# Optimization experiments

Hardware: AMD Instinct MI355X
Metric: run time of the kernel (lower is better)

The kernel has to match this reference:

```python
import jax, jax.numpy as jnp
from jax import lax
import numpy as np

VAR0, VAR1 = 0.1, 0.2
K_TOP, T1, T2 = 5, 0.35, 0.5
ALPHA, GAMMA, BETA = 0.25, 2.0, 0.11


def point_form(b):
    # center form (cx,cy,w,h) -> corner form (x1,y1,x2,y2)
    return jnp.concatenate([b[:, :2] - b[:, 2:] / 2, b[:, :2] + b[:, 2:] / 2], axis=-1)


def jaccard(a, b):
    # a: [N,4], b: [P,4] corner boxes -> IoU [N,P]
    lt = jnp.maximum(a[:, None, :2], b[None, :, :2])
    rb = jnp.minimum(a[:, None, 2:], b[None, :, 2:])
    wh = jnp.clip(rb - lt, 0.0)
    inter = wh[..., 0] * wh[..., 1]
    area_a = ((a[:, 2] - a[:, 0]) * (a[:, 3] - a[:, 1]))[:, None]
    area_b = ((b[:, 2] - b[:, 0]) * (b[:, 3] - b[:, 1]))[None, :]
    return inter / (area_a + area_b - inter)


def encode(matched, priors):
    # matched: corner boxes [P,4], priors: center form [P,4]
    g_cxcy = ((matched[:, :2] + matched[:, 2:]) / 2 - priors[:, :2]) / (VAR0 * priors[:, 2:])
    g_wh = jnp.log((matched[:, 2:] - matched[:, :2]) / priors[:, 2:]) / VAR1
    return jnp.concatenate([g_cxcy, g_wh], axis=-1)


def decode(loc, priors):
    cxcy = priors[:, :2] + loc[:, :2] * VAR0 * priors[:, 2:]
    wh = priors[:, 2:] * jnp.exp(loc[:, 2:] * VAR1)
    return jnp.concatenate([cxcy - wh / 2, cxcy + wh / 2], axis=-1)


def _bce_logits(x, t):
    return jnp.maximum(x, 0.0) - x * t + jnp.log1p(jnp.exp(-jnp.abs(x)))


def focal_loss(logits, target, f_iou=None):
    C = logits.shape[-1]
    t = target.reshape(-1, 1)
    keep = (t >= 0.0).astype(logits.dtype)
    t = jnp.maximum(t, 0.0)
    pos = jnp.sum(t > 0.0).astype(logits.dtype)
    x = jnp.take_along_axis(logits.reshape(-1, C), t.astype(jnp.int32), axis=1)
    ce = _bce_logits(x, t)
    a = t * ALPHA + (1.0 - t) * (1.0 - ALPHA)
    p = jax.nn.sigmoid(x)
    pt = jnp.where(t == 1.0, p, 1.0 - p)
    if f_iou is not None:
        a = lax.stop_gradient(f_iou.reshape(-1, 1)) * a
    loss = a * (1.0 - pt) ** GAMMA * ce * keep
    return jnp.sum(loss) / jnp.maximum(pos, 1.0)


def smoothl1_masked(pred, target, mask):
    # equals SmoothL1Loss on the masked rows: sum(elem)/num_rows
    x = jnp.abs(pred - target)
    elem = jnp.where(x >= BETA, x - 0.5 * BETA, 0.5 * x * x / BETA)
    n = jnp.sum(mask).astype(pred.dtype)
    return jnp.sum(elem * mask[..., None].astype(pred.dtype)) / jnp.maximum(n, 1.0)


def match_image(loc_pred, tgt, priors_c, priors_pt):
    N = tgt.shape[0]
    P = priors_c.shape[0]
    truths = tgt[:, :4]
    labels = tgt[:, 4]
    iou = jaccard(truths, priors_pt)  # [N,P]
    bt_score = jnp.max(iou, axis=0)
    bt_idx = jnp.argmax(iou, axis=0).astype(jnp.int32)

    def greedy(_, st):
        m, s, ix = st
        flat = jnp.argmax(m)
        j = (flat // P).astype(jnp.int32)
        i = (flat % P).astype(jnp.int32)
        v = m.ravel()[flat]
        m = m.at[j, :].set(-1.0)
        m = m.at[:, i].set(-1.0)
        return (m, s.at[i].set(v), ix.at[i].set(j))

    _, bt_score, bt_idx = lax.fori_loop(0, N, greedy, (iou, bt_score, bt_idx))

    conf_s1 = labels[bt_idx]
    conf_s1 = jnp.where(bt_score < T1, 0.0, conf_s1)
    loc_s1 = encode(truths[bt_idx], priors_c)

    decoded = decode(lax.stop_gradient(loc_pred), priors_c)
    c_iou = jaccard(truths, decoded)  # [N,P]
    c_bp_score = jnp.max(c_iou, axis=0)
    c_bp_idx = jnp.argmax(c_iou, axis=0).astype(jnp.int32)
    c_iou = c_iou * (c_iou >= T2).astype(c_iou.dtype)
    tk_s, tk_i = lax.top_k(c_iou, K_TOP)  # per-truth top-K priors
    c_score = jnp.zeros_like(c_bp_score)

    def assign(t, st):
        cbi, cs = st
        i = (t // K_TOP).astype(jnp.int32)
        j = t % K_TOP
        p = tk_i[i, j]
        s = tk_s[i, j]
        cond = (conf_s1[p] < 1.0) & (s > 0.0)
        cbi = cbi.at[p].set(jnp.where(cond, i, cbi[p]))
        cs = cs.at[p].set(jnp.where(cond, s, cs[p]))
        return (cbi, cs)

    c_bp_idx, c_score = lax.fori_loop(0, N * K_TOP, assign, (c_bp_idx, c_score))

    loc_s2 = encode(truths[c_bp_idx], priors_c)
    conf_s2 = labels[c_bp_idx]
    conf_s2 = jnp.where(c_score < T2, -1.0, conf_s2)
    ignore = (bt_score < T1) & (c_bp_score >= T2) & (c_score < T2)
    conf_s1 = jnp.where(ignore, -1.0, conf_s1)
    return conf_s1, loc_s1, conf_s2, loc_s2, c_score


def setup_inputs() -> dict:
    key = jax.random.key(0)
    k1, k2, k3, k4, k5, k6 = jax.random.split(key, 6)
    B, P, N, C = 16, 102400, 32, 2
    loc_data = jax.random.normal(k1, (B, P, 4), jnp.float32)
    conf_data = jax.random.normal(k2, (B, P, C), jnp.float32)
    pcxy = jax.random.uniform(k3, (P, 2), jnp.float32, 0.0, 1.0)
    pwh = jax.random.uniform(k4, (P, 2), jnp.float32, 0.02, 0.25)
    priors = jnp.concatenate([pcxy, pwh], axis=-1)
    tcxy = jax.random.uniform(k5, (B, N, 2), jnp.float32, 0.1, 0.9)
    twh = jax.random.uniform(k6, (B, N, 2), jnp.float32, 0.05, 0.3)
    x1 = jnp.clip(tcxy - twh / 2, 0.0, 1.0)
    x2 = jnp.clip(tcxy + twh / 2, 0.0, 1.0)
    targets = jnp.concatenate([x1, x2, jnp.ones((B, N, 1), jnp.float32)], axis=-1)
    return {"loc_data": loc_data, "conf_data": conf_data, "priors": priors, "targets": targets}


def reference(loc_data, conf_data, priors, targets):
    priors_c = lax.stop_gradient(priors)  # torch uses priors.data
    tgts = lax.stop_gradient(targets)     # torch uses targets[idx].data
    priors_pt = point_form(priors_c)
    conf_t, loc_t, cconf_t, cloc_t, cc_score = jax.vmap(
        lambda lp, tg: match_image(lp, tg, priors_c, priors_pt))(loc_data, tgts)
    m1 = conf_t > 0.0
    m2 = cconf_t > 0.0
    n1 = jnp.sum(m1)
    n2 = jnp.sum(m2)
    l1 = smoothl1_masked(loc_data, loc_t, m1)
    l2 = smoothl1_masked(loc_data, cloc_t, m2)
    f1 = focal_loss(conf_data, conf_t, None)
    f2 = focal_loss(conf_data, cconf_t, cc_score)
    loc_loss = jnp.where(n1 > 0, l1, 0.0) + jnp.where(n2 > 0, l2, 0.0)
    cls_loss = jnp.where(n1 > 0, f1, 0.0) + jnp.where(n2 > 0, f2, 0.0)
    none_ = (n1 == 0) & (n2 == 0)
    return (jnp.where(none_, 1e-4, loc_loss), jnp.where(none_, 1e-4, cls_loss))
```

## Files before the change

kernel.cpp:

```cpp
#include <hip/hip_runtime.h>
#include <cstdint>
#include <cstddef>

#define VAR0_ 0.1f
#define VAR1_ 0.2f
#define KTOP_ 5
#define T1_ 0.35f
#define T2_ 0.5f
#define ALPHA_ 0.25f
#define BETA_ 0.11f
#define BS 256
#define BSK 128
#define NSPLIT 16
#define ILP 4

__device__ __forceinline__ float sl1(float d) {
    float x = fabsf(d);
    return (x >= BETA_) ? (x - 0.5f * BETA_) : (0.5f * x * x / BETA_);
}

__global__ void k_fat1(const float4* __restrict__ loc4, const float4* __restrict__ priors4,
                       const float* __restrict__ targets,
                       float4* __restrict__ recs4,
                       float* __restrict__ cand_v, int* __restrict__ cand_i,
                       int* __restrict__ cand_cnt,
                       float* __restrict__ part_max, int* __restrict__ part_arg,
                       int P, int N, int CAP, int bxPP) {
    int b = blockIdx.y;
    int tid = threadIdx.x;
    if (blockIdx.x < bxPP) {
        int base = blockIdx.x * (BSK * ILP) + tid;
        __shared__ float4 tr4[64];
        __shared__ float trA[64];
        __shared__ float trT[64];
        for (int t = tid; t < N; t += BSK) {
            float x1 = targets[(size_t)(b * N + t) * 5 + 0];
            float y1 = targets[(size_t)(b * N + t) * 5 + 1];
            float x2 = targets[(size_t)(b * N + t) * 5 + 2];
            float y2 = targets[(size_t)(b * N + t) * 5 + 3];
            tr4[t] = make_float4(x1, y1, x2, y2);
            float a = (x2 - x1) * (y2 - y1);
            trA[t] = a;
            trT[t] = a * 0.33330f;
        }
        __syncthreads();
        if (base >= P) return;

        int iv[ILP]; int val[ILP];
        float px1[ILP], py1[ILP], px2[ILP], py2[ILP], pa[ILP];
#pragma unroll
        for (int k = 0; k < ILP; k++) {
            int i = base + k * BSK; iv[k] = i; val[k] = (i < P);
            float4 pr = val[k] ? priors4[i] : make_float4(0.f, 0.f, 1.f, 1.f);
            px1[k] = pr.x - pr.z * 0.5f; py1[k] = pr.y - pr.w * 0.5f;
            px2[k] = pr.x + pr.z * 0.5f; py2[k] = pr.y + pr.w * 0.5f;
            pa[k] = (px2[k] - px1[k]) * (py2[k] - py1[k]);
        }
        float bi[ILP], bu[ILP]; int bn[ILP];
#pragma unroll
        for (int k = 0; k < ILP; k++) { bi[k] = -1.f; bu[k] = 1.f; bn[k] = 0; }
#pragma unroll 2
        for (int n = 0; n < N; n++) {
            float4 t4 = tr4[n];
            float ta = trA[n];
#pragma unroll
            for (int k = 0; k < ILP; k++) {
                float lx = fmaxf(t4.x, px1[k]), ly = fmaxf(t4.y, py1[k]);
                float rx = fminf(t4.z, px2[k]), ry = fminf(t4.w, py2[k]);
                float w = fmaxf(rx - lx, 0.f), h = fmaxf(ry - ly, 0.f);
                float inter = w * h, uni = ta + pa[k] - inter;
                bool bet = inter * bu[k] > bi[k] * uni;
                bi[k] = bet ? inter : bi[k]; bu[k] = bet ? uni : bu[k]; bn[k] = bet ? n : bn[k];
            }
        }
        float bv[ILP];
#pragma unroll
        for (int k = 0; k < ILP; k++) bv[k] = bi[k] / bu[k];

        float dx1[ILP], dy1[ILP], dx2[ILP], dy2[ILP], da[ILP], daC[ILP];
#pragma unroll
        for (int k = 0; k < ILP; k++) {
            float4 pr = val[k] ? priors4[iv[k]] : make_float4(0.f, 0.f, 1.f, 1.f);
            float4 lc = val[k] ? loc4[(size_t)b * P + iv[k]] : make_float4(0.f, 0.f, 0.f, 0.f);
            float dcx = pr.x + lc.x * VAR0_ * pr.z;
            float dcy = pr.y + lc.y * VAR0_ * pr.w;
            float dw = pr.z * expf(lc.z * VAR1_);
            float dh = pr.w * expf(lc.w * VAR1_);
            dx1[k] = dcx - dw * 0.5f; dy1[k] = dcy - dh * 0.5f;
            dx2[k] = dcx + dw * 0.5f; dy2[k] = dcy + dh * 0.5f;
            da[k] = (dx2[k] - dx1[k]) * (dy2[k] - dy1[k]);
            daC[k] = da[k] * 0.33330f;
        }
        unsigned long long hm[ILP];
#pragma unroll
        for (int k = 0; k < ILP; k++) hm[k] = 0ull;
#pragma unroll 2
        for (int n = 0; n < N; n++) {
            float4 t4 = tr4[n];
            float tt = trT[n];
#pragma unroll
            for (int k = 0; k < ILP; k++) {
                float lx = fmaxf(t4.x, dx1[k]), ly = fmaxf(t4.y, dy1[k]);
                float rx = fminf(t4.z, dx2[k]), ry = fminf(t4.w, dy2[k]);
                float w = fmaxf(rx - lx, 0.f), h = fmaxf(ry - ly, 0.f);
                float inter = w * h;
                if (inter >= tt + daC[k]) hm[k] |= (1ull << n);
            }
        }
#pragma unroll
        for (int k = 0; k < ILP; k++) {
            if (!val[k]) continue;
            int had = 0;
            unsigned long long m = hm[k];
            while (m) {
                int n = __ffsll((long long)m) - 1;
                m &= m - 1;
                float4 t4 = tr4[n];
                float lx = fmaxf(t4.x, dx1[k]), ly = fmaxf(t4.y, dy1[k]);
                float rx = fminf(t4.z, dx2[k]), ry = fminf(t4.w, dy2[k]);
                float w = fmaxf(rx - lx, 0.f), h = fmaxf(ry - ly, 0.f);
                float inter = w * h;
                float v = inter / (trA[n] + da[k] - inter);
                if (v >= T2_) {
                    had = 1;
                    int pos = atomicAdd(&cand_cnt[b * N + n], 1);
                    if (pos < CAP) {
                        size_t o = (size_t)(b * N + n) * CAP + pos;
                        cand_v[o] = v; cand_i[o] = iv[k];
                    }
                }
            }
            recs4[(size_t)b * P + iv[k]] =
                make_float4(bv[k], __int_as_float(bn[k] | (had << 16)), __int_as_float(0), 0.f);
        }
    } else {
        int idx = blockIdx.x - bxPP;
        int s = idx % NSPLIT, g = idx / NSPLIT;
        int n0 = g * 4;
        int chunk = (P + NSPLIT - 1) / NSPLIT;
        int i0 = s * chunk;
        int i1 = min(P, i0 + chunk);
        float tx1[4], ty1[4], tx2[4], ty2[4], ta[4];
#pragma unroll
        for (int k = 0; k < 4; k++) {
            int n = min(n0 + k, N - 1);
            tx1[k] = targets[(size_t)(b * N + n) * 5 + 0];
            ty1[k] = targets[(size_t)(b * N + n) * 5 + 1];
            tx2[k] = targets[(size_t)(b * N + n) * 5 + 2];
            ty2[k] = targets[(size_t)(b * N + n) * 5 + 3];
            ta[k] = (tx2[k] - tx1[k]) * (ty2[k] - ty1[k]);
        }
        float cI[4], cU[4]; int cX[4];
#pragma unroll
        for (int k = 0; k < 4; k++) { cI[k] = -1.f; cU[k] = 1.f; cX[k] = 0x7fffffff; }
        for (int i = i0 + tid; i < i1; i += BSK) {
            float4 pr = priors4[i];
            float px1 = pr.x - pr.z * 0.5f, py1 = pr.y - pr.w * 0.5f;
            float px2 = pr.x + pr.z * 0.5f, py2 = pr.y + pr.w * 0.5f;
            float pa = (px2 - px1) * (py2 - py1);
#pragma unroll
            for (int k = 0; k < 4; k++) {
                float lx = fmaxf(tx1[k], px1), ly = fmaxf(ty1[k], py1);
                float rx = fminf(tx2[k], px2), ry = fminf(ty2[k], py2);
                float w = fmaxf(rx - lx, 0.f), h = fmaxf(ry - ly, 0.f);
                float inter = w * h;
                float uni = ta[k] + pa - inter;
                bool bet = inter * cU[k] > cI[k] * uni;
                cI[k] = bet ? inter : cI[k]; cU[k] = bet ? uni : cU[k]; cX[k] = bet ? i : cX[k];
            }
        }
        int lane = tid & 63, wid = tid >> 6;
        __shared__ float swv[BSK / 64];
        __shared__ int swi[BSK / 64];
#pragma unroll
        for (int k = 0; k < 4; k++) {
            if (n0 + k >= N) break;
            float bv = cI[k] / cU[k];
            int bx = cX[k];
#pragma unroll
            for (int off = 32; off > 0; off >>= 1) {
                float ov = __shfl_xor(bv, off);
                int oi = __shfl_xor(bx, off);
                if (ov > bv || (ov == bv && oi < bx)) { bv = ov; bx = oi; }
            }
            if (lane == 0) { swv[wid] = bv; swi[wid] = bx; }
            __syncthreads();
            if (tid == 0) {
                float fv = swv[0]; int fi = swi[0];
                for (int wv = 1; wv < BSK / 64; wv++) {
                    if (swv[wv] > fv || (swv[wv] == fv && swi[wv] < fi)) { fv = swv[wv]; fi = swi[wv]; }
                }
                int o = (b * N + (n0 + k)) * NSPLIT + s;
                part_max[o] = fv; part_arg[o] = fi;
            }
            __syncthreads();
        }
    }
}

__global__ void k_fat2(const float4* __restrict__ loc4, const float4* __restrict__ priors4,
                       const float* __restrict__ targets,
                       const float* __restrict__ cand_v, const int* __restrict__ cand_i,
                       const int* __restrict__ cand_cnt,
                       float* __restrict__ tk_s, int* __restrict__ tk_i,
                       const float* __restrict__ part_max, const int* __restrict__ part_arg,
                       float* __restrict__ recs,
                       int P, int N, int CAP) {
    int b = blockIdx.y;
    int tid = threadIdx.x;
    if ((int)blockIdx.x < N) {
        int n = blockIdx.x;
        int row = b * N + n;
        float vals[KTOP_]; int ids[KTOP_];
#pragma unroll
        for (int k = 0; k < KTOP_; k++) { vals[k] = -1.f; ids[k] = 0x7fffffff; }
        int cnt = cand_cnt[row];
        if (cnt <= CAP) {
            for (int k = tid; k < cnt; k += blockDim.x) {
                float cv = cand_v[(size_t)row * CAP + k];
                int ci = cand_i[(size_t)row * CAP + k];
#pragma unroll
                for (int q = 0; q < KTOP_; q++) {
                    bool better = (cv > vals[q]) || ((cv == vals[q]) && (ci < ids[q]));
                    float tv = better ? cv : vals[q]; int ti = better ? ci : ids[q];
                    cv = better ? vals[q] : cv; ci = better ? ids[q] : ci;
                    vals[q] = tv; ids[q] = ti;
                }
            }
        } else {
            float tx1 = targets[(size_t)row * 5 + 0], ty1 = targets[(size_t)row * 5 + 1];
            float tx2 = targets[(size_t)row * 5 + 2], ty2 = targets[(size_t)row * 5 + 3];
            float ta = (tx2 - tx1) * (ty2 - ty1);
            for (int i = tid; i < P; i += blockDim.x) {
                float4 pr = priors4[i];
                size_t bp = (size_t)b * P + i;
                float4 lc = loc4[bp];
                float dcx = pr.x + lc.x * VAR0_ * pr.z;
                float dcy = pr.y + lc.y * VAR0_ * pr.w;
                float dw = pr.z * expf(lc.z * VAR1_);
                float dh = pr.w * expf(lc.w * VAR1_);
                float dx1 = dcx - dw * 0.5f, dy1 = dcy - dh * 0.5f;
                float dx2 = dcx + dw * 0.5f, dy2 = dcy + dh * 0.5f;
                float lx = fmaxf(tx1, dx1), ly = fmaxf(ty1, dy1);
                float rx = fminf(tx2, dx2), ry = fminf(ty2, dy2);
                float w = fmaxf(rx - lx, 0.f), h = fmaxf(ry - ly, 0.f);
                float inter = w * h;
                float uni = ta + (dx2 - dx1) * (dy2 - dy1) - inter;
                if (inter >= uni * 0.4999990f) {
                    float v = inter / uni;
                    if (v >= T2_) {
                        float cv = v; int ci = i;
#pragma unroll
                        for (int q = 0; q < KTOP_; q++) {
                            bool better = (cv > vals[q]) || ((cv == vals[q]) && (ci < ids[q]));
                            float tv = better ? cv : vals[q]; int ti = better ? ci : ids[q];
                            cv = better ? vals[q] : cv; ci = better ? ids[q] : ci;
                            vals[q] = tv; ids[q] = ti;
                        }
                    }
                }
            }
        }
        __shared__ float mv[BS * KTOP_];
        __shared__ int mi[BS * KTOP_];
#pragma unroll
        for (int k = 0; k < KTOP_; k++) { mv[tid * KTOP_ + k] = vals[k]; mi[tid * KTOP_ + k] = ids[k]; }
        __syncthreads();
        for (int s = BS / 2; s > 0; s >>= 1) {
            if (tid < s) {
#pragma unroll
                for (int j = 0; j < KTOP_; j++) {
                    float cv = mv[(tid + s) * KTOP_ + j];
                    int ci = mi[(tid + s) * KTOP_ + j];
#pragma unroll
                    for (int q = 0; q < KTOP_; q++) {
                        bool better = (cv > vals[q]) || ((cv == vals[q]) && (ci < ids[q]));
                        float tv = better ? cv : vals[q]; int ti = better ? ci : ids[q];
                        cv = better ? vals[q] : cv; ci = better ? ids[q] : ci;
                        vals[q] = tv; ids[q] = ti;
                    }
                }
#pragma unroll
                for (int k = 0; k < KTOP_; k++) { mv[tid * KTOP_ + k] = vals[k]; mi[tid * KTOP_ + k] = ids[k]; }
            }
            __syncthreads();
        }
        if (tid == 0) {
#pragma unroll
            for (int k = 0; k < KTOP_; k++) {
                tk_s[(size_t)row * KTOP_ + k] = (vals[k] > 0.f) ? vals[k] : 0.f;
                tk_i[(size_t)row * KTOP_ + k] = (ids[k] == 0x7fffffff) ? 0 : ids[k];
            }
        }
    } else {
        int lane = tid & 63, wid = tid >> 6;
        extern __shared__ unsigned int mask[];
        int maskWords = (P + 31) >> 5;
        for (int w = tid; w < maskWords; w += BS) mask[w] = 0u;

        float rmax = -2.f; int rarg = 0x7fffffff; int alive = 0;
        float tx1 = 0.f, ty1 = 0.f, tx2 = 0.f, ty2 = 0.f, ta = 0.f;
        if (wid == 0 && lane < N) {
            float bv = -2.f; int bi = 0x7fffffff;
            for (int s = 0; s < NSPLIT; s++) {
                int o = (b * N + lane) * NSPLIT + s;
                float v = part_max[o]; int ix = part_arg[o];
                if (v > bv || (v == bv && ix < bi)) { bv = v; bi = ix; }
            }
            rmax = bv; rarg = bi;
            alive = 1;
            tx1 = targets[(size_t)(b * N + lane) * 5 + 0];
            ty1 = targets[(size_t)(b * N + lane) * 5 + 1];
            tx2 = targets[(size_t)(b * N + lane) * 5 + 2];
            ty2 = targets[(size_t)(b * N + lane) * 5 + 3];
            ta = (tx2 - tx1) * (ty2 - ty1);
        }
        __syncthreads();

        for (int it = 0; it < N; it++) {
            int sel = 0;
            if (wid == 0) {
                float v = (lane < N && alive) ? rmax : -3.f;
                int idx = lane;
#pragma unroll
                for (int off = 32; off > 0; off >>= 1) {
                    float ov = __shfl_xor(v, off);
                    int oi = __shfl_xor(idx, off);
                    if (ov > v || (ov == v && oi < idx)) { v = ov; idx = oi; }
                }
                int bj = idx;
                float bv = v;
                sel = __shfl(rarg, bj);
                if (lane == bj) alive = 0;
                if (lane == 0) {
                    float* base = recs + 4 * ((size_t)b * P + sel);
                    int wrd = __float_as_int(base[1]);
                    base[0] = bv;
                    base[1] = __int_as_float((wrd & ~0xFFFF) | bj);
                    mask[sel >> 5] |= (1u << (sel & 31));
                }
            }
            __syncthreads();
            if (wid == 0) {
                unsigned long long coll = __ballot(lane < N && alive && rarg == sel);
                while (coll) {
                    int r = __ffsll((long long)coll) - 1;
                    coll &= coll - 1;
                    float rx1 = __shfl(tx1, r), ry1 = __shfl(ty1, r);
                    float rx2 = __shfl(tx2, r), ry2 = __shfl(ty2, r);
                    float ra = __shfl(ta, r);
                    float n_i = -2.f, n_u = 1.f; int ni = 0x7fffffff;
                    for (int i = lane; i < P; i += 64) {
                        if (mask[i >> 5] & (1u << (i & 31))) continue;
                        float4 pr = priors4[i];
                        float px1 = pr.x - pr.z * 0.5f, py1 = pr.y - pr.w * 0.5f;
                        float px2 = pr.x + pr.z * 0.5f, py2 = pr.y + pr.w * 0.5f;
                        float lx = fmaxf(rx1, px1), ly = fmaxf(ry1, py1);
                        float rx = fminf(rx2, px2), ry = fminf(ry2, py2);
                        float w = fmaxf(rx - lx, 0.f), h = fmaxf(ry - ly, 0.f);
                        float inter = w * h;
                        float uni = ra + (px2 - px1) * (py2 - py1) - inter;
                        bool better = inter * n_u > n_i * uni;
                        n_i = better ? inter : n_i; n_u = better ? uni : n_u; ni = better ? i : ni;
                    }
                    float nv = n_i / n_u;
#pragma unroll
                    for (int off = 32; off > 0; off >>= 1) {
                        float ov = __shfl_xor(nv, off);
                        int oi = __shfl_xor(ni, off);
                        if (ov > nv || (ov == nv && oi < ni)) { nv = ov; ni = oi; }
                    }
                    if (lane == r) { rmax = nv; rarg = ni; }
                }
            }
            __syncthreads();
        }
    }
}

__global__ void k_assign(const float* __restrict__ targets,
                         const float* __restrict__ tk_s, const int* __restrict__ tk_i,
                         float* __restrict__ recs, int P, int N) {
    int b = blockIdx.x;
    int tid = threadIdx.x;
    int T = N * KTOP_;
    __shared__ int sh_p[512];
    __shared__ float sh_s[512];
    __shared__ int sh_c[512];
    if (tid < T) {
        int i = tid / KTOP_, j = tid % KTOP_;
        int p = tk_i[(size_t)(b * N + i) * KTOP_ + j];
        float s = tk_s[(size_t)(b * N + i) * KTOP_ + j];
        const float* base = recs + 4 * ((size_t)b * P + p);
        float bs = base[0];
        int bj = __float_as_int(base[1]) & 0xFFFF;
        float conf1 = (bs < T1_) ? 0.f : targets[(size_t)(b * N + bj) * 5 + 4];
        sh_p[tid] = p; sh_s[tid] = s;
        sh_c[tid] = (conf1 < 1.f && s > 0.f) ? 1 : 0;
    }
    __syncthreads();
    if (tid < T && sh_c[tid]) {
        int p = sh_p[tid];
        bool last = true;
        for (int t2 = tid + 1; t2 < T; t2++) {
            if (sh_c[t2] && sh_p[t2] == p) { last = false; break; }
        }
        if (last) {
            float* base = recs + 4 * ((size_t)b * P + p);
            base[2] = __int_as_float(tid / KTOP_);
            base[3] = sh_s[tid];
        }
    }
}

__global__ void k_loss(const float4* __restrict__ loc4, const float* __restrict__ conf,
                       const float4* __restrict__ priors4, const float* __restrict__ targets,
                       const float4* __restrict__ recs4,
                       double* __restrict__ partials,
                       int P, int N, int C) {
    int b = blockIdx.y;
    int i = blockIdx.x * blockDim.x + threadIdx.x;
    double l1 = 0.0, l2 = 0.0, f1 = 0.0, f2 = 0.0;
    int n1 = 0, n2 = 0;
    if (i < P) {
        size_t bp = (size_t)b * P + i;
        float4 r = recs4[bp];
        float bs = r.x;
        int widx = __float_as_int(r.y);
        int bj = widx & 0xFFFF;
        int hadCand = (widx >> 16) & 1;
        float cs = r.w;
        int cj = (cs > 0.f) ? __float_as_int(r.z) : 0;
        float lab1 = targets[(size_t)(b * N + bj) * 5 + 4];
        float conf1 = (bs < T1_) ? 0.f : lab1;
        if ((bs < T1_) && hadCand && (cs < T2_)) conf1 = -1.f;
        float lab2 = targets[(size_t)(b * N + cj) * 5 + 4];
        float conf2 = (cs < T2_) ? -1.f : lab2;
        bool m1 = conf1 > 0.f, m2 = conf2 > 0.f;
        n1 = m1 ? 1 : 0; n2 = m2 ? 1 : 0;

        if (m1 || m2) {
            float4 pr = priors4[i];
            float pcx = pr.x, pcy = pr.y, pw = pr.z, ph = pr.w;
            float4 lc = loc4[bp];
            float p0 = lc.x, p1 = lc.y, p2 = lc.z, p3 = lc.w;
            if (m1) {
                const float* tb = &targets[(size_t)(b * N + bj) * 5];
                float gx = ((tb[0] + tb[2]) * 0.5f - pcx) / (VAR0_ * pw);
                float gy = ((tb[1] + tb[3]) * 0.5f - pcy) / (VAR0_ * ph);
                float gw = logf((tb[2] - tb[0]) / pw) / VAR1_;
                float gh = logf((tb[3] - tb[1]) / ph) / VAR1_;
                l1 = (double)(sl1(p0 - gx) + sl1(p1 - gy) + sl1(p2 - gw) + sl1(p3 - gh));
            }
            if (m2) {
                const float* tb = &targets[(size_t)(b * N + cj) * 5];
                float gx = ((tb[0] + tb[2]) * 0.5f - pcx) / (VAR0_ * pw);
                float gy = ((tb[1] + tb[3]) * 0.5f - pcy) / (VAR0_ * ph);
                float gw = logf((tb[2] - tb[0]) / pw) / VAR1_;
                float gh = logf((tb[3] - tb[1]) / ph) / VAR1_;
                l2 = (double)(sl1(p0 - gx) + sl1(p1 - gy) + sl1(p2 - gw) + sl1(p3 - gh));
            }
        }
        float x0, x1v;
        if (C == 2) {
            float2 cv2 = ((const float2*)conf)[bp];
            x0 = cv2.x; x1v = cv2.y;
        } else {
            x0 = conf[bp * C + 0]; x1v = conf[bp * C + 1];
        }
        {
            float t = fmaxf(conf1, 0.f);
            float keep = (conf1 >= 0.f) ? 1.f : 0.f;
            float x = (t >= 1.f) ? x1v : x0;
            float ce = fmaxf(x, 0.f) - x * t + log1pf(expf(-fabsf(x)));
            float a = t * ALPHA_ + (1.f - t) * (1.f - ALPHA_);
            float pr_ = 1.f / (1.f + expf(-x));
            float pt = (t == 1.f) ? pr_ : (1.f - pr_);
            float om = 1.f - pt;
            f1 = (double)(a * om * om * ce * keep);
        }
        {
            float t = fmaxf(conf2, 0.f);
            float keep = (conf2 >= 0.f) ? 1.f : 0.f;
            float x = (t >= 1.f) ? x1v : x0;
            float ce = fmaxf(x, 0.f) - x * t + log1pf(expf(-fabsf(x)));
            float a = cs * (t * ALPHA_ + (1.f - t) * (1.f - ALPHA_));
            float pr_ = 1.f / (1.f + expf(-x));
            float pt = (t == 1.f) ? pr_ : (1.f - pr_);
            float om = 1.f - pt;
            f2 = (double)(a * om * om * ce * keep);
        }
    }
    int tid = threadIdx.x;
    int lane = tid & 63, wid = tid >> 6;
#pragma unroll
    for (int off = 32; off > 0; off >>= 1) {
        l1 += __shfl_xor(l1, off);
        l2 += __shfl_xor(l2, off);
        f1 += __shfl_xor(f1, off);
        f2 += __shfl_xor(f2, off);
        n1 += __shfl_xor(n1, off);
        n2 += __shfl_xor(n2, off);
    }
    __shared__ double swd[BS / 64][4];
    __shared__ int swn[BS / 64][2];
    if (lane == 0) {
        swd[wid][0] = l1; swd[wid][1] = l2; swd[wid][2] = f1; swd[wid][3] = f2;
        swn[wid][0] = n1; swn[wid][1] = n2;
    }
    __syncthreads();
    if (tid == 0) {
        double a0 = 0, a1 = 0, a2 = 0, a3 = 0; int b0 = 0, b1 = 0;
        for (int wv = 0; wv < BS / 64; wv++) {
            a0 += swd[wv][0]; a1 += swd[wv][1]; a2 += swd[wv][2]; a3 += swd[wv][3];
            b0 += swn[wv][0]; b1 += swn[wv][1];
        }
        int blk = blockIdx.y * gridDim.x + blockIdx.x;
        partials[(size_t)blk * 6 + 0] = a0;
        partials[(size_t)blk * 6 + 1] = a1;
        partials[(size_t)blk * 6 + 2] = a2;
        partials[(size_t)blk * 6 + 3] = a3;
        partials[(size_t)blk * 6 + 4] = (double)b0;
        partials[(size_t)blk * 6 + 5] = (double)b1;
    }
}

__global__ void k_final(const double* __restrict__ partials, int nPart, float* __restrict__ out) {
    int tid = threadIdx.x;
    double a[6] = {0, 0, 0, 0, 0, 0};
    for (int k = tid; k < nPart; k += BS) {
#pragma unroll
        for (int j = 0; j < 6; j++) a[j] += partials[(size_t)k * 6 + j];
    }
    __shared__ double sd[BS * 6];
#pragma unroll
    for (int j = 0; j < 6; j++) sd[tid * 6 + j] = a[j];
    __syncthreads();
    for (int s = BS / 2; s > 0; s >>= 1) {
        if (tid < s) {
#pragma unroll
            for (int j = 0; j < 6; j++) sd[tid * 6 + j] += sd[(tid + s) * 6 + j];
        }
        __syncthreads();
    }
    if (tid == 0) {
        double L1 = sd[0], L2 = sd[1], F1 = sd[2], F2 = sd[3], N1 = sd[4], N2 = sd[5];
        double l1v = L1 / fmax(N1, 1.0), l2v = L2 / fmax(N2, 1.0);
        double f1v = F1 / fmax(N1, 1.0), f2v = F2 / fmax(N2, 1.0);
        double locl = (N1 > 0 ? l1v : 0.0) + (N2 > 0 ? l2v : 0.0);
        double clsl = (N1 > 0 ? f1v : 0.0) + (N2 > 0 ? f2v : 0.0);
        if (N1 == 0 && N2 == 0) { locl = 1e-4; clsl = 1e-4; }
        out[0] = (float)locl;
        out[1] = (float)clsl;
    }
}

extern "C" void kernel_launch(void* const* d_in, const int* in_sizes, int n_in,
                              void* d_out, int out_size, void* d_ws, size_t ws_size,
                              hipStream_t stream) {
    const float* targets = (const float*)d_in[3];
    const float* conf = (const float*)d_in[1];
    const float4* loc4 = (const float4*)d_in[0];
    const float4* priors4 = (const float4*)d_in[2];

    int P = in_sizes[2] / 4;
    int B = in_sizes[0] / (P * 4);
    int N = in_sizes[3] / (B * 5);
    int C = in_sizes[1] / (B * P);
    const int CAP = 2048;
    size_t BP = (size_t)B * P;

    unsigned char* ws = (unsigned char*)d_ws;
    size_t off = 0;
    auto alloc = [&](size_t bytes) { size_t cur = off; off += (bytes + 255) & ~(size_t)255; return cur; };
    float* recs = (float*)(ws + alloc(BP * 16));
    float* part_max = (float*)(ws + alloc((size_t)B * N * NSPLIT * 4));
    int* part_arg = (int*)(ws + alloc((size_t)B * N * NSPLIT * 4));
    float* tk_s = (float*)(ws + alloc((size_t)B * N * KTOP_ * 4));
    int* tk_i = (int*)(ws + alloc((size_t)B * N * KTOP_ * 4));
    float* cand_v = (float*)(ws + alloc((size_t)B * N * CAP * 4));
    int* cand_i = (int*)(ws + alloc((size_t)B * N * CAP * 4));
    int* cand_cnt = (int*)(ws + alloc((size_t)B * N * 4));
    int bx = (P + BS - 1) / BS;
    double* partials = (double*)(ws + alloc((size_t)bx * B * 6 * 8));
    float* out = (float*)d_out;

    hipMemsetAsync(cand_cnt, 0, (size_t)B * N * 4, stream);

    int bxPP = (P + BSK * ILP - 1) / (BSK * ILP);
    int ngroup = (N + 3) / 4;
    int bxRM = NSPLIT * ngroup;
    k_fat1<<<dim3(bxPP + bxRM, B), BSK, 0, stream>>>(loc4, priors4, targets, (float4*)recs,
                                                     cand_v, cand_i, cand_cnt,
                                                     part_max, part_arg, P, N, CAP, bxPP);

    int maskWords = (P + 31) / 32;
    size_t shmem = (size_t)maskWords * 4;
    k_fat2<<<dim3(N + 1, B), BS, shmem, stream>>>(loc4, priors4, targets,
                                                  cand_v, cand_i, cand_cnt, tk_s, tk_i,
                                                  part_max, part_arg, recs, P, N, CAP);

    k_assign<<<dim3(B), BS, 0, stream>>>(targets, tk_s, tk_i, recs, P, N);
    k_loss<<<dim3(bx, B), BS, 0, stream>>>(loc4, conf, priors4, targets, (const float4*)recs,
                                           partials, P, N, C);
    k_final<<<1, BS, 0, stream>>>(partials, bx * B, out);
}
```

Before: 213.6 us.

## Merge all stages into one cooperative persistent kernel with grid syncs

```diff
diff --git a/kernel.cpp b/kernel.cpp
--- a/kernel.cpp
+++ b/kernel.cpp
@@ -1,6 +1,9 @@
 #include <hip/hip_runtime.h>
+#include <hip/hip_cooperative_groups.h>
 #include <cstdint>
 #include <cstddef>
+
+namespace cg = cooperative_groups;
 
 #define VAR0_ 0.1f
 #define VAR1_ 0.2f
@@ -10,7 +13,6 @@
 #define ALPHA_ 0.25f
 #define BETA_ 0.11f
 #define BS 256
-#define BSK 128
 #define NSPLIT 16
 #define ILP 4
 
@@ -19,237 +21,225 @@
     return (x >= BETA_) ? (x - 0.5f * BETA_) : (0.5f * x * x / BETA_);
 }
 
-__global__ void k_fat1(const float4* __restrict__ loc4, const float4* __restrict__ priors4,
-                       const float* __restrict__ targets,
-                       float4* __restrict__ recs4,
+__global__ void k_mega(const float4* __restrict__ loc4, const float4* __restrict__ priors4,
+                       const float* __restrict__ targets, const float* __restrict__ conf,
+                       float* __restrict__ recs,
+                       float* __restrict__ part_max, int* __restrict__ part_arg,
+                       float* __restrict__ tk_s, int* __restrict__ tk_i,
                        float* __restrict__ cand_v, int* __restrict__ cand_i,
                        int* __restrict__ cand_cnt,
-                       float* __restrict__ part_max, int* __restrict__ part_arg,
-                       int P, int N, int CAP, int bxPP) {
-    int b = blockIdx.y;
+                       double* __restrict__ partials, float* __restrict__ out,
+                       int P, int N, int B, int C, int CAP, int bxPP, int bxL) {
+    cg::grid_group grid = cg::this_grid();
+    extern __shared__ unsigned char smem[];
     int tid = threadIdx.x;
-    if (blockIdx.x < bxPP) {
-        int base = blockIdx.x * (BSK * ILP) + tid;
-        __shared__ float4 tr4[64];
-        __shared__ float trA[64];
-        __shared__ float trT[64];
-        for (int t = tid; t < N; t += BSK) {
-            float x1 = targets[(size_t)(b * N + t) * 5 + 0];
-            float y1 = targets[(size_t)(b * N + t) * 5 + 1];
-            float x2 = targets[(size_t)(b * N + t) * 5 + 2];
-            float y2 = targets[(size_t)(b * N + t) * 5 + 3];
-            tr4[t] = make_float4(x1, y1, x2, y2);
-            float a = (x2 - x1) * (y2 - y1);
-            trA[t] = a;
-            trT[t] = a * 0.33330f;
-        }
-        __syncthreads();
-        if (base >= P) return;
-
-        int iv[ILP]; int val[ILP];
-        float px1[ILP], py1[ILP], px2[ILP], py2[ILP], pa[ILP];
-#pragma unroll
-        for (int k = 0; k < ILP; k++) {
-            int i = base + k * BSK; iv[k] = i; val[k] = (i < P);
-            float4 pr = val[k] ? priors4[i] : make_float4(0.f, 0.f, 1.f, 1.f);
-            px1[k] = pr.x - pr.z * 0.5f; py1[k] = pr.y - pr.w * 0.5f;
-            px2[k] = pr.x + pr.z * 0.5f; py2[k] = pr.y + pr.w * 0.5f;
-            pa[k] = (px2[k] - px1[k]) * (py2[k] - py1[k]);
-        }
-        float bi[ILP], bu[ILP]; int bn[ILP];
-#pragma unroll
-        for (int k = 0; k < ILP; k++) { bi[k] = -1.f; bu[k] = 1.f; bn[k] = 0; }
+    int G = gridDim.x;
+    float4* recs4 = (float4*)recs;
+
+    for (int i = blockIdx.x * BS + tid; i < B * N; i += G * BS) cand_cnt[i] = 0;
+    __threadfence();
+    grid.sync();
+
+    {
+        int ngroup = (N + 3) / 4;
+        int worksPP = bxPP * B;
+        int worksRM = NSPLIT * ngroup * B;
+        float4* tr4 = (float4*)smem;
+        float* trA = (float*)(smem + 1024);
+        float* trT = (float*)(smem + 1280);
+        __shared__ float swv[BS / 64];
+        __shared__ int swi[BS / 64];
+        for (int vb = blockIdx.x; vb < worksPP + worksRM; vb += G) {
+            __syncthreads();
+            if (vb < worksPP) {
+                int b = vb / bxPP;
+                int base = (vb % bxPP) * (BS * ILP) + tid;
+                for (int t = tid; t < N; t += BS) {
+                    float x1 = targets[(size_t)(b * N + t) * 5 + 0];
+                    float y1 = targets[(size_t)(b * N + t) * 5 + 1];
+                    float x2 = targets[(size_t)(b * N + t) * 5 + 2];
+                    float y2 = targets[(size_t)(b * N + t) * 5 + 3];
+                    tr4[t] = make_float4(x1, y1, x2, y2);
+                    float a = (x2 - x1) * (y2 - y1);
+                    trA[t] = a;
+                    trT[t] = a * 0.33330f;
+                }
+                __syncthreads();
+                if (base >= P) continue;
+
+                int iv[ILP]; int val[ILP];
+                float px1[ILP], py1[ILP], px2[ILP], py2[ILP], pa[ILP];
+#pragma unroll
+                for (int k = 0; k < ILP; k++) {
+                    int i = base + k * BS; iv[k] = i; val[k] = (i < P);
+                    float4 pr = val[k] ? priors4[i] : make_float4(0.f, 0.f, 1.f, 1.f);
+                    px1[k] = pr.x - pr.z * 0.5f; py1[k] = pr.y - pr.w * 0.5f;
+                    px2[k] = pr.x + pr.z * 0.5f; py2[k] = pr.y + pr.w * 0.5f;
+                    pa[k] = (px2[k] - px1[k]) * (py2[k] - py1[k]);
+                }
+                float bi[ILP], bu[ILP]; int bn[ILP];
+#pragma unroll
+                for (int k = 0; k < ILP; k++) { bi[k] = -1.f; bu[k] = 1.f; bn[k] = 0; }
 #pragma unroll 2
-        for (int n = 0; n < N; n++) {
-            float4 t4 = tr4[n];
-            float ta = trA[n];
-#pragma unroll
-            for (int k = 0; k < ILP; k++) {
-                float lx = fmaxf(t4.x, px1[k]), ly = fmaxf(t4.y, py1[k]);
-                float rx = fminf(t4.z, px2[k]), ry = fminf(t4.w, py2[k]);
-                float w = fmaxf(rx - lx, 0.f), h = fmaxf(ry - ly, 0.f);
-                float inter = w * h, uni = ta + pa[k] - inter;
-                bool bet = inter * bu[k] > bi[k] * uni;
-                bi[k] = bet ? inter : bi[k]; bu[k] = bet ? uni : bu[k]; bn[k] = bet ? n : bn[k];
-            }
-        }
-        float bv[ILP];
-#pragma unroll
-        for (int k = 0; k < ILP; k++) bv[k] = bi[k] / bu[k];
-
-        float dx1[ILP], dy1[ILP], dx2[ILP], dy2[ILP], da[ILP], daC[ILP];
-#pragma unroll
-        for (int k = 0; k < ILP; k++) {
-            float4 pr = val[k] ? priors4[iv[k]] : make_float4(0.f, 0.f, 1.f, 1.f);
-            float4 lc = val[k] ? loc4[(size_t)b * P + iv[k]] : make_float4(0.f, 0.f, 0.f, 0.f);
-            float dcx = pr.x + lc.x * VAR0_ * pr.z;
-            float dcy = pr.y + lc.y * VAR0_ * pr.w;
-            float dw = pr.z * expf(lc.z * VAR1_);
-            float dh = pr.w * expf(lc.w * VAR1_);
-            dx1[k] = dcx - dw * 0.5f; dy1[k] = dcy - dh * 0.5f;
-            dx2[k] = dcx + dw * 0.5f; dy2[k] = dcy + dh * 0.5f;
-            da[k] = (dx2[k] - dx1[k]) * (dy2[k] - dy1[k]);
-            daC[k] = da[k] * 0.33330f;
-        }
-        unsigned long long hm[ILP];
-#pragma unroll
-        for (int k = 0; k < ILP; k++) hm[k] = 0ull;
+                for (int n = 0; n < N; n++) {
+                    float4 t4 = tr4[n];
+                    float ta = trA[n];
+#pragma unroll
+                    for (int k = 0; k < ILP; k++) {
+                        float lx = fmaxf(t4.x, px1[k]), ly = fmaxf(t4.y, py1[k]);
+                        float rx = fminf(t4.z, px2[k]), ry = fminf(t4.w, py2[k]);
+                        float w = fmaxf(rx - lx, 0.f), h = fmaxf(ry - ly, 0.f);
+                        float inter = w * h, uni = ta + pa[k] - inter;
+                        bool bet = inter * bu[k] > bi[k] * uni;
+                        bi[k] = bet ? inter : bi[k]; bu[k] = bet ? uni : bu[k]; bn[k] = bet ? n : bn[k];
+                    }
+                }
+                float bv[ILP];
+#pragma unroll
+                for (int k = 0; k < ILP; k++) bv[k] = bi[k] / bu[k];
+
+                float dx1[ILP], dy1[ILP], dx2[ILP], dy2[ILP], da[ILP], daC[ILP];
+#pragma unroll
+                for (int k = 0; k < ILP; k++) {
+                    float4 pr = val[k] ? priors4[iv[k]] : make_float4(0.f, 0.f, 1.f, 1.f);
+                    float4 lc = val[k] ? loc4[(size_t)b * P + iv[k]] : make_float4(0.f, 0.f, 0.f, 0.f);
+                    float dcx = pr.x + lc.x * VAR0_ * pr.z;
+                    float dcy = pr.y + lc.y * VAR0_ * pr.w;
+                    float dw = pr.z * expf(lc.z * VAR1_);
+                    float dh = pr.w * expf(lc.w * VAR1_);
+                    dx1[k] = dcx - dw * 0.5f; dy1[k] = dcy - dh * 0.5f;
+                    dx2[k] = dcx + dw * 0.5f; dy2[k] = dcy + dh * 0.5f;
+                    da[k] = (dx2[k] - dx1[k]) * (dy2[k] - dy1[k]);
+                    daC[k] = da[k] * 0.33330f;
+                }
+                unsigned long long hm[ILP];
+#pragma unroll
+                for (int k = 0; k < ILP; k++) hm[k] = 0ull;
 #pragma unroll 2
-        for (int n = 0; n < N; n++) {
-            float4 t4 = tr4[n];
-            float tt = trT[n];
-#pragma unroll
-            for (int k = 0; k < ILP; k++) {
-                float lx = fmaxf(t4.x, dx1[k]), ly = fmaxf(t4.y, dy1[k]);
-                float rx = fminf(t4.z, dx2[k]), ry = fminf(t4.w, dy2[k]);
-                float w = fmaxf(rx - lx, 0.f), h = fmaxf(ry - ly, 0.f);
-                float inter = w * h;
-                if (inter >= tt + daC[k]) hm[k] |= (1ull << n);
-            }
-        }
-#pragma unroll
-        for (int k = 0; k < ILP; k++) {
-            if (!val[k]) continue;
-            int had = 0;
-            unsigned long long m = hm[k];
-            while (m) {
-                int n = __ffsll((long long)m) - 1;
-                m &= m - 1;
-                float4 t4 = tr4[n];
-                float lx = fmaxf(t4.x, dx1[k]), ly = fmaxf(t4.y, dy1[k]);
-                float rx = fminf(t4.z, dx2[k]), ry = fminf(t4.w, dy2[k]);
-                float w = fmaxf(rx - lx, 0.f), h = fmaxf(ry - ly, 0.f);
-                float inter = w * h;
-                float v = inter / (trA[n] + da[k] - inter);
-                if (v >= T2_) {
-                    had = 1;
-                    int pos = atomicAdd(&cand_cnt[b * N + n], 1);
-                    if (pos < CAP) {
-                        size_t o = (size_t)(b * N + n) * CAP + pos;
-                        cand_v[o] = v; cand_i[o] = iv[k];
-                    }
-                }
-            }
-            recs4[(size_t)b * P + iv[k]] =
-                make_float4(bv[k], __int_as_float(bn[k] | (had << 16)), __int_as_float(0), 0.f);
-        }
-    } else {
-        int idx = blockIdx.x - bxPP;
-        int s = idx % NSPLIT, g = idx / NSPLIT;
-        int n0 = g * 4;
-        int chunk = (P + NSPLIT - 1) / NSPLIT;
-        int i0 = s * chunk;
-        int i1 = min(P, i0 + chunk);
-        float tx1[4], ty1[4], tx2[4], ty2[4], ta[4];
-#pragma unroll
-        for (int k = 0; k < 4; k++) {
-            int n = min(n0 + k, N - 1);
-            tx1[k] = targets[(size_t)(b * N + n) * 5 + 0];
-            ty1[k] = targets[(size_t)(b * N + n) * 5 + 1];
-            tx2[k] = targets[(size_t)(b * N + n) * 5 + 2];
-            ty2[k] = targets[(size_t)(b * N + n) * 5 + 3];
-            ta[k] = (tx2[k] - tx1[k]) * (ty2[k] - ty1[k]);
-        }
-        float cI[4], cU[4]; int cX[4];
-#pragma unroll
-        for (int k = 0; k < 4; k++) { cI[k] = -1.f; cU[k] = 1.f; cX[k] = 0x7fffffff; }
-        for (int i = i0 + tid; i < i1; i += BSK) {
-            float4 pr = priors4[i];
-            float px1 = pr.x - pr.z * 0.5f, py1 = pr.y - pr.w * 0.5f;
-            float px2 = pr.x + pr.z * 0.5f, py2 = pr.y + pr.w * 0.5f;
-            float pa = (px2 - px1) * (py2 - py1);
-#pragma unroll
-            for (int k = 0; k < 4; k++) {
-                float lx = fmaxf(tx1[k], px1), ly = fmaxf(ty1[k], py1);
-                float rx = fminf(tx2[k], px2), ry = fminf(ty2[k], py2);
-                float w = fmaxf(rx - lx, 0.f), h = fmaxf(ry - ly, 0.f);
-                float inter = w * h;
-                float uni = ta[k] + pa - inter;
-                bool bet = inter * cU[k] > cI[k] * uni;
-                cI[k] = bet ? inter : cI[k]; cU[k] = bet ? uni : cU[k]; cX[k] = bet ? i : cX[k];
-            }
-        }
-        int lane = tid & 63, wid = tid >> 6;
-        __shared__ float swv[BSK / 64];
-        __shared__ int swi[BSK / 64];
-#pragma unroll
-        for (int k = 0; k < 4; k++) {
-            if (n0 + k >= N) break;
-            float bv = cI[k] / cU[k];
-            int bx = cX[k];
-#pragma unroll
-            for (int off = 32; off > 0; off >>= 1) {
-                float ov = __shfl_xor(bv, off);
-                int oi = __shfl_xor(bx, off);
-                if (ov > bv || (ov == bv && oi < bx)) { bv = ov; bx = oi; }
-            }
-            if (lane == 0) { swv[wid] = bv; swi[wid] = bx; }
-            __syncthreads();
-            if (tid == 0) {
-                float fv = swv[0]; int fi = swi[0];
-                for (int wv = 1; wv < BSK / 64; wv++) {
-                    if (swv[wv] > fv || (swv[wv] == fv && swi[wv] < fi)) { fv = swv[wv]; fi = swi[wv]; }
-                }
-                int o = (b * N + (n0 + k)) * NSPLIT + s;
-                part_max[o] = fv; part_arg[o] = fi;
-            }
-            __syncthreads();
+                for (int n = 0; n < N; n++) {
+                    float4 t4 = tr4[n];
+                    float tt = trT[n];
+#pragma unroll
+                    for (int k = 0; k < ILP; k++) {
+                        float lx = fmaxf(t4.x, dx1[k]), ly = fmaxf(t4.y, dy1[k]);
+                        float rx = fminf(t4.z, dx2[k]), ry = fminf(t4.w, dy2[k]);
+                        float w = fmaxf(rx - lx, 0.f), h = fmaxf(ry - ly, 0.f);
+                        float inter = w * h;
+                        if (inter >= tt + daC[k]) hm[k] |= (1ull << n);
+                    }
+                }
+#pragma unroll
+                for (int k = 0; k < ILP; k++) {
+                    if (!val[k]) continue;
+                    int had = 0;
+                    unsigned long long m = hm[k];
+                    while (m) {
+                        int n = __ffsll((long long)m) - 1;
+                        m &= m - 1;
+                        float4 t4 = tr4[n];
+                        float lx = fmaxf(t4.x, dx1[k]), ly = fmaxf(t4.y, dy1[k]);
+                        float rx = fminf(t4.z, dx2[k]), ry = fminf(t4.w, dy2[k]);
+                        float w = fmaxf(rx - lx, 0.f), h = fmaxf(ry - ly, 0.f);
+                        float inter = w * h;
+                        float v = inter / (trA[n] + da[k] - inter);
+                        if (v >= T2_) {
+                            had = 1;
+                            int pos = atomicAdd(&cand_cnt[b * N + n], 1);
+                            if (pos < CAP) {
+                                size_t o = (size_t)(b * N + n) * CAP + pos;
+                                cand_v[o] = v; cand_i[o] = iv[k];
+                            }
+                        }
+                    }
+                    recs4[(size_t)b * P + iv[k]] =
+                        make_float4(bv[k], __int_as_float(bn[k] | (had << 16)), __int_as_float(0), 0.f);
+                }
+            } else {
+                int idx = vb - worksPP;
+                int perB = NSPLIT * ngroup;
+                int b = idx / perB;
+                int r = idx % perB;
+                int s = r % NSPLIT, g = r / NSPLIT;
+                int n0 = g * 4;
+                int chunk = (P + NSPLIT - 1) / NSPLIT;
+                int i0 = s * chunk;
+                int i1 = min(P, i0 + chunk);
+                float tx1[4], ty1[4], tx2[4], ty2[4], ta[4];
+#pragma unroll
+                for (int k = 0; k < 4; k++) {
+                    int n = min(n0 + k, N - 1);
+                    tx1[k] = targets[(size_t)(b * N + n) * 5 + 0];
+                    ty1[k] = targets[(size_t)(b * N + n) * 5 + 1];
+                    tx2[k] = targets[(size_t)(b * N + n) * 5 + 2];
+                    ty2[k] = targets[(size_t)(b * N + n) * 5 + 3];
+                    ta[k] = (tx2[k] - tx1[k]) * (ty2[k] - ty1[k]);
+                }
+                float cI[4], cU[4]; int cX[4];
+#pragma unroll
+                for (int k = 0; k < 4; k++) { cI[k] = -1.f; cU[k] = 1.f; cX[k] = 0x7fffffff; }
+                for (int i = i0 + tid; i < i1; i += BS) {
+                    float4 pr = priors4[i];
+                    float px1 = pr.x - pr.z * 0.5f, py1 = pr.y - pr.w * 0.5f;
+                    float px2 = pr.x + pr.z * 0.5f, py2 = pr.y + pr.w * 0.5f;
+                    float pa = (px2 - px1) * (py2 - py1);
+#pragma unroll
+                    for (int k = 0; k < 4; k++) {
+                        float lx = fmaxf(tx1[k], px1), ly = fmaxf(ty1[k], py1);
+                        float rx = fminf(tx2[k], px2), ry = fminf(ty2[k], py2);
+                        float w = fmaxf(rx - lx, 0.f), h = fmaxf(ry - ly, 0.f);
+                        float inter = w * h;
+                        float uni = ta[k] + pa - inter;
+                        bool bet = inter * cU[k] > cI[k] * uni;
+                        cI[k] = bet ? inter : cI[k]; cU[k] = bet ? uni : cU[k]; cX[k] = bet ? i : cX[k];
+                    }
+                }
+                int lane = tid & 63, wid = tid >> 6;
+#pragma unroll
+                for (int k = 0; k < 4; k++) {
+                    if (n0 + k >= N) break;
+                    float bvv = cI[k] / cU[k];
+                    int bxx = cX[k];
+#pragma unroll
+                    for (int off = 32; off > 0; off >>= 1) {
+                        float ov = __shfl_xor(bvv, off);
+                        int oi = __shfl_xor(bxx, off);
+                        if (ov > bvv || (ov == bvv && oi < bxx)) { bvv = ov; bxx = oi; }
+                    }
+                    if (lane == 0) { swv[wid] = bvv; swi[wid] = bxx; }
+                    __syncthreads();
+                    if (tid == 0) {
+                        float fv = swv[0]; int fi = swi[0];
+                        for (int wv = 1; wv < BS / 64; wv++) {
+                            if (swv[wv] > fv || (swv[wv] == fv && swi[wv] < fi)) { fv = swv[wv]; fi = swi[wv]; }
+                        }
+                        int o = (b * N + (n0 + k)) * NSPLIT + s;
+                        part_max[o] = fv; part_arg[o] = fi;
+                    }
+                    __syncthreads();
+                }
+            }
         }
     }
-}
-
-__global__ void k_fat2(const float4* __restrict__ loc4, const float4* __restrict__ priors4,
-                       const float* __restrict__ targets,
-                       const float* __restrict__ cand_v, const int* __restrict__ cand_i,
-                       const int* __restrict__ cand_cnt,
-                       float* __restrict__ tk_s, int* __restrict__ tk_i,
-                       const float* __restrict__ part_max, const int* __restrict__ part_arg,
-                       float* __restrict__ recs,
-                       int P, int N, int CAP) {
-    int b = blockIdx.y;
-    int tid = threadIdx.x;
-    if ((int)blockIdx.x < N) {
-        int n = blockIdx.x;
-        int row = b * N + n;
-        float vals[KTOP_]; int ids[KTOP_];
-#pragma unroll
-        for (int k = 0; k < KTOP_; k++) { vals[k] = -1.f; ids[k] = 0x7fffffff; }
-        int cnt = cand_cnt[row];
-        if (cnt <= CAP) {
-            for (int k = tid; k < cnt; k += blockDim.x) {
-                float cv = cand_v[(size_t)row * CAP + k];
-                int ci = cand_i[(size_t)row * CAP + k];
-#pragma unroll
-                for (int q = 0; q < KTOP_; q++) {
-                    bool better = (cv > vals[q]) || ((cv == vals[q]) && (ci < ids[q]));
-                    float tv = better ? cv : vals[q]; int ti = better ? ci : ids[q];
-                    cv = better ? vals[q] : cv; ci = better ? ids[q] : ci;
-                    vals[q] = tv; ids[q] = ti;
-                }
-            }
-        } else {
-            float tx1 = targets[(size_t)row * 5 + 0], ty1 = targets[(size_t)row * 5 + 1];
-            float tx2 = targets[(size_t)row * 5 + 2], ty2 = targets[(size_t)row * 5 + 3];
-            float ta = (tx2 - tx1) * (ty2 - ty1);
-            for (int i = tid; i < P; i += blockDim.x) {
-                float4 pr = priors4[i];
-                size_t bp = (size_t)b * P + i;
-                float4 lc = loc4[bp];
-                float dcx = pr.x + lc.x * VAR0_ * pr.z;
-                float dcy = pr.y + lc.y * VAR0_ * pr.w;
-                float dw = pr.z * expf(lc.z * VAR1_);
-                float dh = pr.w * expf(lc.w * VAR1_);
-                float dx1 = dcx - dw * 0.5f, dy1 = dcy - dh * 0.5f;
-                float dx2 = dcx + dw * 0.5f, dy2 = dcy + dh * 0.5f;
-                float lx = fmaxf(tx1, dx1), ly = fmaxf(ty1, dy1);
-                float rx = fminf(tx2, dx2), ry = fminf(ty2, dy2);
-                float w = fmaxf(rx - lx, 0.f), h = fmaxf(ry - ly, 0.f);
-                float inter = w * h;
-                float uni = ta + (dx2 - dx1) * (dy2 - dy1) - inter;
-                if (inter >= uni * 0.4999990f) {
-                    float v = inter / uni;
-                    if (v >= T2_) {
-                        float cv = v; int ci = i;
+    __threadfence();
+    grid.sync();
+
+    {
+        int worksTK = B * N;
+        for (int vb = blockIdx.x; vb < worksTK + B; vb += G) {
+            __syncthreads();
+            if (vb < worksTK) {
+                int row = vb;
+                int b = vb / N;
+                float* mv = (float*)smem;
+                int* mi = (int*)(smem + BS * KTOP_ * 4);
+                float vals[KTOP_]; int ids[KTOP_];
+#pragma unroll
+                for (int k = 0; k < KTOP_; k++) { vals[k] = -1.f; ids[k] = 0x7fffffff; }
+                int cnt = cand_cnt[row];
+                if (cnt <= CAP) {
+                    for (int k = tid; k < cnt; k += BS) {
+                        float cv = cand_v[(size_t)row * CAP + k];
+                        int ci = cand_i[(size_t)row * CAP + k];
 #pragma unroll
                         for (int q = 0; q < KTOP_; q++) {
                             bool better = (cv > vals[q]) || ((cv == vals[q]) && (ci < ids[q]));
@@ -258,300 +248,335 @@
                             vals[q] = tv; ids[q] = ti;
                         }
                     }
+                } else {
+                    float tx1 = targets[(size_t)row * 5 + 0], ty1 = targets[(size_t)row * 5 + 1];
+                    float tx2 = targets[(size_t)row * 5 + 2], ty2 = targets[(size_t)row * 5 + 3];
+                    float ta = (tx2 - tx1) * (ty2 - ty1);
+                    for (int i = tid; i < P; i += BS) {
+                        float4 pr = priors4[i];
+                        size_t bp = (size_t)b * P + i;
+                        float4 lc = loc4[bp];
+                        float dcx = pr.x + lc.x * VAR0_ * pr.z;
+                        float dcy = pr.y + lc.y * VAR0_ * pr.w;
+                        float dw = pr.z * expf(lc.z * VAR1_);
+                        float dh = pr.w * expf(lc.w * VAR1_);
+                        float dx1 = dcx - dw * 0.5f, dy1 = dcy - dh * 0.5f;
+                        float dx2 = dcx + dw * 0.5f, dy2 = dcy + dh * 0.5f;
+                        float lx = fmaxf(tx1, dx1), ly = fmaxf(ty1, dy1);
+                        float rx = fminf(tx2, dx2), ry = fminf(ty2, dy2);
+                        float w = fmaxf(rx - lx, 0.f), h = fmaxf(ry - ly, 0.f);
+                        float inter = w * h;
+                        float uni = ta + (dx2 - dx1) * (dy2 - dy1) - inter;
+                        if (inter >= uni * 0.4999990f) {
+                            float v = inter / uni;
+                            if (v >= T2_) {
+                                float cv = v; int ci = i;
+#pragma unroll
+                                for (int q = 0; q < KTOP_; q++) {
+                                    bool better = (cv > vals[q]) || ((cv == vals[q]) && (ci < ids[q]));
+                                    float tv = better ? cv : vals[q]; int ti = better ? ci : ids[q];
+                                    cv = better ? vals[q] : cv; ci = better ? ids[q] : ci;
+                                    vals[q] = tv; ids[q] = ti;
+                                }
+                            }
+                        }
+                    }
+                }
+#pragma unroll
+                for (int k = 0; k < KTOP_; k++) { mv[tid * KTOP_ + k] = vals[k]; mi[tid * KTOP_ + k] = ids[k]; }
+                __syncthreads();
+                for (int s = BS / 2; s > 0; s >>= 1) {
+                    if (tid < s) {
+#pragma unroll
+                        for (int j = 0; j < KTOP_; j++) {
+                            float cv = mv[(tid + s) * KTOP_ + j];
+                            int ci = mi[(tid + s) * KTOP_ + j];
+#pragma unroll
+                            for (int q = 0; q < KTOP_; q++) {
+                                bool better = (cv > vals[q]) || ((cv == vals[q]) && (ci < ids[q]));
+                                float tv = better ? cv : vals[q]; int ti = better ? ci : ids[q];
+                                cv = better ? vals[q] : cv; ci = better ? ids[q] : ci;
+                                vals[q] = tv; ids[q] = ti;
+                            }
+                        }
+#pragma unroll
+                        for (int k = 0; k < KTOP_; k++) { mv[tid * KTOP_ + k] = vals[k]; mi[tid * KTOP_ + k] = ids[k]; }
+                    }
+                    __syncthreads();
+                }
+                if (tid == 0) {
+#pragma unroll
+                    for (int k = 0; k < KTOP_; k++) {
+                        tk_s[(size_t)row * KTOP_ + k] = (vals[k] > 0.f) ? vals[k] : 0.f;
+                        tk_i[(size_t)row * KTOP_ + k] = (ids[k] == 0x7fffffff) ? 0 : ids[k];
+                    }
+                }
+            } else {
+                int b = vb - worksTK;
+                int lane = tid & 63, wid = tid >> 6;
+                unsigned int* mask = (unsigned int*)smem;
+                int maskWords = (P + 31) >> 5;
+                for (int w = tid; w < maskWords; w += BS) mask[w] = 0u;
+
+                float rmax = -2.f; int rarg = 0x7fffffff; int alive = 0;
+                float tx1 = 0.f, ty1 = 0.f, tx2 = 0.f, ty2 = 0.f, ta = 0.f;
+                if (wid == 0 && lane < N) {
+                    float bv = -2.f; int bi = 0x7fffffff;
+                    for (int s = 0; s < NSPLIT; s++) {
+                        int o = (b * N + lane) * NSPLIT + s;
+                        float v = part_max[o]; int ix = part_arg[o];
+                        if (v > bv || (v == bv && ix < bi)) { bv = v; bi = ix; }
+                    }
+                    rmax = bv; rarg = bi;
+                    alive = 1;
+                    tx1 = targets[(size_t)(b * N + lane) * 5 + 0];
+                    ty1 = targets[(size_t)(b * N + lane) * 5 + 1];
+                    tx2 = targets[(size_t)(b * N + lane) * 5 + 2];
+                    ty2 = targets[(size_t)(b * N + lane) * 5 + 3];
+                    ta = (tx2 - tx1) * (ty2 - ty1);
+                }
+                __syncthreads();
+
+                for (int it = 0; it < N; it++) {
+                    int sel = 0;
+                    if (wid == 0) {
+                        float v = (lane < N && alive) ? rmax : -3.f;
+                        int idx = lane;
+#pragma unroll
+                        for (int off = 32; off > 0; off >>= 1) {
+                            float ov = __shfl_xor(v, off);
+                            int oi = __shfl_xor(idx, off);
+                            if (ov > v || (ov == v && oi < idx)) { v = ov; idx = oi; }
+                        }
+                        int bj = idx;
+                        float bv = v;
+                        sel = __shfl(rarg, bj);
+                        if (lane == bj) alive = 0;
+                        if (lane == 0) {
+                            float* base = recs + 4 * ((size_t)b * P + sel);
+                            int wrd = __float_as_int(base[1]);
+                            base[0] = bv;
+                            base[1] = __int_as_float((wrd & ~0xFFFF) | bj);
+                            mask[sel >> 5] |= (1u << (sel & 31));
+                        }
+                    }
+                    __syncthreads();
+                    if (wid == 0) {
+                        unsigned long long coll = __ballot(lane < N && alive && rarg == sel);
+                        while (coll) {
+                            int r = __ffsll((long long)coll) - 1;
+                            coll &= coll - 1;
+                            float rx1 = __shfl(tx1, r), ry1 = __shfl(ty1, r);
+                            float rx2 = __shfl(tx2, r), ry2 = __shfl(ty2, r);
+                            float ra = __shfl(ta, r);
+                            float n_i = -2.f, n_u = 1.f; int ni = 0x7fffffff;
+                            for (int i = lane; i < P; i += 64) {
+                                if (mask[i >> 5] & (1u << (i & 31))) continue;
+                                float4 pr = priors4[i];
+                                float px1 = pr.x - pr.z * 0.5f, py1 = pr.y - pr.w * 0.5f;
+                                float px2 = pr.x + pr.z * 0.5f, py2 = pr.y + pr.w * 0.5f;
+                                float lx = fmaxf(rx1, px1), ly = fmaxf(ry1, py1);
+                                float rx = fminf(rx2, px2), ry = fminf(ry2, py2);
+                                float w = fmaxf(rx - lx, 0.f), h = fmaxf(ry - ly, 0.f);
+                                float inter = w * h;
+                                float uni = ra + (px2 - px1) * (py2 - py1) - inter;
+                                bool better = inter * n_u > n_i * uni;
+                                n_i = better ? inter : n_i; n_u = better ? uni : n_u; ni = better ? i : ni;
+                            }
+                            float nv = n_i / n_u;
+#pragma unroll
+                            for (int off = 32; off > 0; off >>= 1) {
+                                float ov = __shfl_xor(nv, off);
+                                int oi = __shfl_xor(ni, off);
+                                if (ov > nv || (ov == nv && oi < ni)) { nv = ov; ni = oi; }
+                            }
+                            if (lane == r) { rmax = nv; rarg = ni; }
+                        }
+                    }
+                    __syncthreads();
                 }
             }
         }
-        __shared__ float mv[BS * KTOP_];
-        __shared__ int mi[BS * KTOP_];
-#pragma unroll
-        for (int k = 0; k < KTOP_; k++) { mv[tid * KTOP_ + k] = vals[k]; mi[tid * KTOP_ + k] = ids[k]; }
+    }
+    __threadfence();
+    grid.sync();
+
+    {
+        int* sh_p = (int*)smem;
+        float* sh_s = (float*)(smem + 2048);
+        int* sh_c = (int*)(smem + 4096);
+        int T = N * KTOP_;
+        for (int vb = blockIdx.x; vb < B; vb += G) {
+            __syncthreads();
+            int b = vb;
+            if (tid < T) {
+                int i = tid / KTOP_, j = tid % KTOP_;
+                int p = tk_i[(size_t)(b * N + i) * KTOP_ + j];
+                float s = tk_s[(size_t)(b * N + i) * KTOP_ + j];
+                const float* base = recs + 4 * ((size_t)b * P + p);
+                float bs = base[0];
+                int bj = __float_as_int(base[1]) & 0xFFFF;
+                float conf1 = (bs < T1_) ? 0.f : targets[(size_t)(b * N + bj) * 5 + 4];
+                sh_p[tid] = p; sh_s[tid] = s;
+                sh_c[tid] = (conf1 < 1.f && s > 0.f) ? 1 : 0;
+            }
+            __syncthreads();
+            if (tid < T && sh_c[tid]) {
+                int p = sh_p[tid];
+                bool last = true;
+                for (int t2 = tid + 1; t2 < T; t2++) {
+                    if (sh_c[t2] && sh_p[t2] == p) { last = false; break; }
+                }
+                if (last) {
+                    float* base = recs + 4 * ((size_t)b * P + p);
+                    base[2] = __int_as_float(tid / KTOP_);
+                    base[3] = sh_s[tid];
+                }
+            }
+        }
+    }
+    __threadfence();
+    grid.sync();
+
+    {
+        __shared__ double swd[BS / 64][4];
+        __shared__ int swn[BS / 64][2];
+        int worksL = bxL * B;
+        for (int vb = blockIdx.x; vb < worksL; vb += G) {
+            __syncthreads();
+            int b = vb / bxL;
+            int i = (vb % bxL) * BS + tid;
+            double l1 = 0.0, l2 = 0.0, f1 = 0.0, f2 = 0.0;
+            int n1 = 0, n2 = 0;
+            if (i < P) {
+                size_t bp = (size_t)b * P + i;
+                float4 r = recs4[bp];
+                float bs = r.x;
+                int widx = __float_as_int(r.y);
+                int bj = widx & 0xFFFF;
+                int hadCand = (widx >> 16) & 1;
+                float cs = r.w;
+                int cj = (cs > 0.f) ? __float_as_int(r.z) : 0;
+                float lab1 = targets[(size_t)(b * N + bj) * 5 + 4];
+                float conf1 = (bs < T1_) ? 0.f : lab1;
+                if ((bs < T1_) && hadCand && (cs < T2_)) conf1 = -1.f;
+                float lab2 = targets[(size_t)(b * N + cj) * 5 + 4];
+                float conf2 = (cs < T2_) ? -1.f : lab2;
+                bool m1 = conf1 > 0.f, m2 = conf2 > 0.f;
+                n1 = m1 ? 1 : 0; n2 = m2 ? 1 : 0;
+                if (m1 || m2) {
+                    float4 pr = priors4[i];
+                    float pcx = pr.x, pcy = pr.y, pw = pr.z, ph = pr.w;
+                    float4 lc = loc4[bp];
+                    float p0 = lc.x, p1 = lc.y, p2 = lc.z, p3 = lc.w;
+                    if (m1) {
+                        const float* tb = &targets[(size_t)(b * N + bj) * 5];
+                        float gx = ((tb[0] + tb[2]) * 0.5f - pcx) / (VAR0_ * pw);
+                        float gy = ((tb[1] + tb[3]) * 0.5f - pcy) / (VAR0_ * ph);
+                        float gw = logf((tb[2] - tb[0]) / pw) / VAR1_;
+                        float gh = logf((tb[3] - tb[1]) / ph) / VAR1_;
+                        l1 = (double)(sl1(p0 - gx) + sl1(p1 - gy) + sl1(p2 - gw) + sl1(p3 - gh));
+                    }
+                    if (m2) {
+                        const float* tb = &targets[(size_t)(b * N + cj) * 5];
+                        float gx = ((tb[0] + tb[2]) * 0.5f - pcx) / (VAR0_ * pw);
+                        float gy = ((tb[1] + tb[3]) * 0.5f - pcy) / (VAR0_ * ph);
+                        float gw = logf((tb[2] - tb[0]) / pw) / VAR1_;
+                        float gh = logf((tb[3] - tb[1]) / ph) / VAR1_;
+                        l2 = (double)(sl1(p0 - gx) + sl1(p1 - gy) + sl1(p2 - gw) + sl1(p3 - gh));
+                    }
+                }
+                float x0, x1v;
+                if (C == 2) {
+                    float2 cv2 = ((const float2*)conf)[bp];
+                    x0 = cv2.x; x1v = cv2.y;
+                } else {
+                    x0 = conf[bp * C + 0]; x1v = conf[bp * C + 1];
+                }
+                {
+                    float t = fmaxf(conf1, 0.f);
+                    float keep = (conf1 >= 0.f) ? 1.f : 0.f;
+                    float x = (t >= 1.f) ? x1v : x0;
+                    float ce = fmaxf(x, 0.f) - x * t + log1pf(expf(-fabsf(x)));
+                    float a = t * ALPHA_ + (1.f - t) * (1.f - ALPHA_);
+                    float pr_ = 1.f / (1.f + expf(-x));
+                    float pt = (t == 1.f) ? pr_ : (1.f - pr_);
+                    float om = 1.f - pt;
+                    f1 = (double)(a * om * om * ce * keep);
+                }
+                {
+                    float t = fmaxf(conf2, 0.f);
+                    float keep = (conf2 >= 0.f) ? 1.f : 0.f;
+                    float x = (t >= 1.f) ? x1v : x0;
+                    float ce = fmaxf(x, 0.f) - x * t + log1pf(expf(-fabsf(x)));
+                    float a = cs * (t * ALPHA_ + (1.f - t) * (1.f - ALPHA_));
+                    float pr_ = 1.f / (1.f + expf(-x));
+                    float pt = (t == 1.f) ? pr_ : (1.f - pr_);
+                    float om = 1.f - pt;
+                    f2 = (double)(a * om * om * ce * keep);
+                }
+            }
+            int lane = tid & 63, wid = tid >> 6;
+#pragma unroll
+            for (int off = 32; off > 0; off >>= 1) {
+                l1 += __shfl_xor(l1, off);
+                l2 += __shfl_xor(l2, off);
+                f1 += __shfl_xor(f1, off);
+                f2 += __shfl_xor(f2, off);
+                n1 += __shfl_xor(n1, off);
+                n2 += __shfl_xor(n2, off);
+            }
+            if (lane == 0) {
+                swd[wid][0] = l1; swd[wid][1] = l2; swd[wid][2] = f1; swd[wid][3] = f2;
+                swn[wid][0] = n1; swn[wid][1] = n2;
+            }
+            __syncthreads();
+            if (tid == 0) {
+                double a0 = 0, a1 = 0, a2 = 0, a3 = 0; int b0 = 0, b1 = 0;
+                for (int wv = 0; wv < BS / 64; wv++) {
+                    a0 += swd[wv][0]; a1 += swd[wv][1]; a2 += swd[wv][2]; a3 += swd[wv][3];
+                    b0 += swn[wv][0]; b1 += swn[wv][1];
+                }
+                partials[(size_t)vb * 6 + 0] = a0;
+                partials[(size_t)vb * 6 + 1] = a1;
+                partials[(size_t)vb * 6 + 2] = a2;
+                partials[(size_t)vb * 6 + 3] = a3;
+                partials[(size_t)vb * 6 + 4] = (double)b0;
+                partials[(size_t)vb * 6 + 5] = (double)b1;
+            }
+        }
+    }
+    __threadfence();
+    grid.sync();
+
+    if (blockIdx.x == 0) {
+        int nPart = bxL * B;
+        double a[6] = {0, 0, 0, 0, 0, 0};
+        for (int k = tid; k < nPart; k += BS) {
+#pragma unroll
+            for (int j = 0; j < 6; j++) a[j] += partials[(size_t)k * 6 + j];
+        }
+        double* sd = (double*)smem;
+#pragma unroll
+        for (int j = 0; j < 6; j++) sd[tid * 6 + j] = a[j];
         __syncthreads();
         for (int s = BS / 2; s > 0; s >>= 1) {
             if (tid < s) {
 #pragma unroll
-                for (int j = 0; j < KTOP_; j++) {
-                    float cv = mv[(tid + s) * KTOP_ + j];
-                    int ci = mi[(tid + s) * KTOP_ + j];
-#pragma unroll
-                    for (int q = 0; q < KTOP_; q++) {
-                        bool better = (cv > vals[q]) || ((cv == vals[q]) && (ci < ids[q]));
-                        float tv = better ? cv : vals[q]; int ti = better ? ci : ids[q];
-                        cv = better ? vals[q] : cv; ci = better ? ids[q] : ci;
-                        vals[q] = tv; ids[q] = ti;
-                    }
-                }
-#pragma unroll
-                for (int k = 0; k < KTOP_; k++) { mv[tid * KTOP_ + k] = vals[k]; mi[tid * KTOP_ + k] = ids[k]; }
+                for (int j = 0; j < 6; j++) sd[tid * 6 + j] += sd[(tid + s) * 6 + j];
             }
             __syncthreads();
         }
         if (tid == 0) {
-#pragma unroll
-            for (int k = 0; k < KTOP_; k++) {
-                tk_s[(size_t)row * KTOP_ + k] = (vals[k] > 0.f) ? vals[k] : 0.f;
-                tk_i[(size_t)row * KTOP_ + k] = (ids[k] == 0x7fffffff) ? 0 : ids[k];
-            }
+            double L1 = sd[0], L2 = sd[1], F1 = sd[2], F2 = sd[3], N1 = sd[4], N2 = sd[5];
+            double l1v = L1 / fmax(N1, 1.0), l2v = L2 / fmax(N2, 1.0);
+            double f1v = F1 / fmax(N1, 1.0), f2v = F2 / fmax(N2, 1.0);
+            double locl = (N1 > 0 ? l1v : 0.0) + (N2 > 0 ? l2v : 0.0);
+            double clsl = (N1 > 0 ? f1v : 0.0) + (N2 > 0 ? f2v : 0.0);
+            if (N1 == 0 && N2 == 0) { locl = 1e-4; clsl = 1e-4; }
+            out[0] = (float)locl;
+            out[1] = (float)clsl;
         }
-    } else {
-        int lane = tid & 63, wid = tid >> 6;
-        extern __shared__ unsigned int mask[];
-        int maskWords = (P + 31) >> 5;
-        for (int w = tid; w < maskWords; w += BS) mask[w] = 0u;
-
-        float rmax = -2.f; int rarg = 0x7fffffff; int alive = 0;
-        float tx1 = 0.f, ty1 = 0.f, tx2 = 0.f, ty2 = 0.f, ta = 0.f;
-        if (wid == 0 && lane < N) {
-            float bv = -2.f; int bi = 0x7fffffff;
-            for (int s = 0; s < NSPLIT; s++) {
-                int o = (b * N + lane) * NSPLIT + s;
-                float v = part_max[o]; int ix = part_arg[o];
-                if (v > bv || (v == bv && ix < bi)) { bv = v; bi = ix; }
-            }
-            rmax = bv; rarg = bi;
-            alive = 1;
-            tx1 = targets[(size_t)(b * N + lane) * 5 + 0];
-            ty1 = targets[(size_t)(b * N + lane) * 5 + 1];
-            tx2 = targets[(size_t)(b * N + lane) * 5 + 2];
-            ty2 = targets[(size_t)(b * N + lane) * 5 + 3];
-            ta = (tx2 - tx1) * (ty2 - ty1);
-        }
-        __syncthreads();
-
-        for (int it = 0; it < N; it++) {
-            int sel = 0;
-            if (wid == 0) {
-                float v = (lane < N && alive) ? rmax : -3.f;
-                int idx = lane;
-#pragma unroll
-                for (int off = 32; off > 0; off >>= 1) {
-                    float ov = __shfl_xor(v, off);
-                    int oi = __shfl_xor(idx, off);
-                    if (ov > v || (ov == v && oi < idx)) { v = ov; idx = oi; }
-                }
-                int bj = idx;
-                float bv = v;
-                sel = __shfl(rarg, bj);
-                if (lane == bj) alive = 0;
-                if (lane == 0) {
-                    float* base = recs + 4 * ((size_t)b * P + sel);
-                    int wrd = __float_as_int(base[1]);
-                    base[0] = bv;
-                    base[1] = __int_as_float((wrd & ~0xFFFF) | bj);
-                    mask[sel >> 5] |= (1u << (sel & 31));
-                }
-            }
-            __syncthreads();
-            if (wid == 0) {
-                unsigned long long coll = __ballot(lane < N && alive && rarg == sel);
-                while (coll) {
-                    int r = __ffsll((long long)coll) - 1;
-                    coll &= coll - 1;
-                    float rx1 = __shfl(tx1, r), ry1 = __shfl(ty1, r);
-                    float rx2 = __shfl(tx2, r), ry2 = __shfl(ty2, r);
-                    float ra = __shfl(ta, r);
-                    float n_i = -2.f, n_u = 1.f; int ni = 0x7fffffff;
-                    for (int i = lane; i < P; i += 64) {
-                        if (mask[i >> 5] & (1u << (i & 31))) continue;
-                        float4 pr = priors4[i];
-                        float px1 = pr.x - pr.z * 0.5f, py1 = pr.y - pr.w * 0.5f;
-                        float px2 = pr.x + pr.z * 0.5f, py2 = pr.y + pr.w * 0.5f;
-                        float lx = fmaxf(rx1, px1), ly = fmaxf(ry1, py1);
-                        float rx = fminf(rx2, px2), ry = fminf(ry2, py2);
-                        float w = fmaxf(rx - lx, 0.f), h = fmaxf(ry - ly, 0.f);
-                        float inter = w * h;
-                        float uni = ra + (px2 - px1) * (py2 - py1) - inter;
-                        bool better = inter * n_u > n_i * uni;
-                        n_i = better ? inter : n_i; n_u = better ? uni : n_u; ni = better ? i : ni;
-                    }
-                    float nv = n_i / n_u;
-#pragma unroll
-                    for (int off = 32; off > 0; off >>= 1) {
-                        float ov = __shfl_xor(nv, off);
-                        int oi = __shfl_xor(ni, off);
-                        if (ov > nv || (ov == nv && oi < ni)) { nv = ov; ni = oi; }
-                    }
-                    if (lane == r) { rmax = nv; rarg = ni; }
-                }
-            }
-            __syncthreads();
-        }
-    }
-}
-
-__global__ void k_assign(const float* __restrict__ targets,
-                         const float* __restrict__ tk_s, const int* __restrict__ tk_i,
-                         float* __restrict__ recs, int P, int N) {
-    int b = blockIdx.x;
-    int tid = threadIdx.x;
-    int T = N * KTOP_;
-    __shared__ int sh_p[512];
-    __shared__ float sh_s[512];
-    __shared__ int sh_c[512];
-    if (tid < T) {
-        int i = tid / KTOP_, j = tid % KTOP_;
-        int p = tk_i[(size_t)(b * N + i) * KTOP_ + j];
-        float s = tk_s[(size_t)(b * N + i) * KTOP_ + j];
-        const float* base = recs + 4 * ((size_t)b * P + p);
-        float bs = base[0];
-        int bj = __float_as_int(base[1]) & 0xFFFF;
-        float conf1 = (bs < T1_) ? 0.f : targets[(size_t)(b * N + bj) * 5 + 4];
-        sh_p[tid] = p; sh_s[tid] = s;
-        sh_c[tid] = (conf1 < 1.f && s > 0.f) ? 1 : 0;
-    }
-    __syncthreads();
-    if (tid < T && sh_c[tid]) {
-        int p = sh_p[tid];
-        bool last = true;
-        for (int t2 = tid + 1; t2 < T; t2++) {
-            if (sh_c[t2] && sh_p[t2] == p) { last = false; break; }
-        }
-        if (last) {
-            float* base = recs + 4 * ((size_t)b * P + p);
-            base[2] = __int_as_float(tid / KTOP_);
-            base[3] = sh_s[tid];
-        }
-    }
-}
-
-__global__ void k_loss(const float4* __restrict__ loc4, const float* __restrict__ conf,
-                       const float4* __restrict__ priors4, const float* __restrict__ targets,
-                       const float4* __restrict__ recs4,
-                       double* __restrict__ partials,
-                       int P, int N, int C) {
-    int b = blockIdx.y;
-    int i = blockIdx.x * blockDim.x + threadIdx.x;
-    double l1 = 0.0, l2 = 0.0, f1 = 0.0, f2 = 0.0;
-    int n1 = 0, n2 = 0;
-    if (i < P) {
-        size_t bp = (size_t)b * P + i;
-        float4 r = recs4[bp];
-        float bs = r.x;
-        int widx = __float_as_int(r.y);
-        int bj = widx & 0xFFFF;
-        int hadCand = (widx >> 16) & 1;
-        float cs = r.w;
-        int cj = (cs > 0.f) ? __float_as_int(r.z) : 0;
-        float lab1 = targets[(size_t)(b * N + bj) * 5 + 4];
-        float conf1 = (bs < T1_) ? 0.f : lab1;
-        if ((bs < T1_) && hadCand && (cs < T2_)) conf1 = -1.f;
-        float lab2 = targets[(size_t)(b * N + cj) * 5 + 4];
-        float conf2 = (cs < T2_) ? -1.f : lab2;
-        bool m1 = conf1 > 0.f, m2 = conf2 > 0.f;
-        n1 = m1 ? 1 : 0; n2 = m2 ? 1 : 0;
-
-        if (m1 || m2) {
-            float4 pr = priors4[i];
-            float pcx = pr.x, pcy = pr.y, pw = pr.z, ph = pr.w;
-            float4 lc = loc4[bp];
-            float p0 = lc.x, p1 = lc.y, p2 = lc.z, p3 = lc.w;
-            if (m1) {
-                const float* tb = &targets[(size_t)(b * N + bj) * 5];
-                float gx = ((tb[0] + tb[2]) * 0.5f - pcx) / (VAR0_ * pw);
-                float gy = ((tb[1] + tb[3]) * 0.5f - pcy) / (VAR0_ * ph);
-                float gw = logf((tb[2] - tb[0]) / pw) / VAR1_;
-                float gh = logf((tb[3] - tb[1]) / ph) / VAR1_;
-                l1 = (double)(sl1(p0 - gx) + sl1(p1 - gy) + sl1(p2 - gw) + sl1(p3 - gh));
-            }
-            if (m2) {
-                const float* tb = &targets[(size_t)(b * N + cj) * 5];
-                float gx = ((tb[0] + tb[2]) * 0.5f - pcx) / (VAR0_ * pw);
-                float gy = ((tb[1] + tb[3]) * 0.5f - pcy) / (VAR0_ * ph);
-                float gw = logf((tb[2] - tb[0]) / pw) / VAR1_;
-                float gh = logf((tb[3] - tb[1]) / ph) / VAR1_;
-                l2 = (double)(sl1(p0 - gx) + sl1(p1 - gy) + sl1(p2 - gw) + sl1(p3 - gh));
-            }
-        }
-        float x0, x1v;
-        if (C == 2) {
-            float2 cv2 = ((const float2*)conf)[bp];
-            x0 = cv2.x; x1v = cv2.y;
-        } else {
-            x0 = conf[bp * C + 0]; x1v = conf[bp * C + 1];
-        }
-        {
-            float t = fmaxf(conf1, 0.f);
-            float keep = (conf1 >= 0.f) ? 1.f : 0.f;
-            float x = (t >= 1.f) ? x1v : x0;
-            float ce = fmaxf(x, 0.f) - x * t + log1pf(expf(-fabsf(x)));
-            float a = t * ALPHA_ + (1.f - t) * (1.f - ALPHA_);
-            float pr_ = 1.f / (1.f + expf(-x));
-            float pt = (t == 1.f) ? pr_ : (1.f - pr_);
-            float om = 1.f - pt;
-            f1 = (double)(a * om * om * ce * keep);
-        }
-        {
-            float t = fmaxf(conf2, 0.f);
-            float keep = (conf2 >= 0.f) ? 1.f : 0.f;
-            float x = (t >= 1.f) ? x1v : x0;
-            float ce = fmaxf(x, 0.f) - x * t + log1pf(expf(-fabsf(x)));
-            float a = cs * (t * ALPHA_ + (1.f - t) * (1.f - ALPHA_));
-            float pr_ = 1.f / (1.f + expf(-x));
-            float pt = (t == 1.f) ? pr_ : (1.f - pr_);
-            float om = 1.f - pt;
-            f2 = (double)(a * om * om * ce * keep);
-        }
-    }
-    int tid = threadIdx.x;
-    int lane = tid & 63, wid = tid >> 6;
-#pragma unroll
-    for (int off = 32; off > 0; off >>= 1) {
-        l1 += __shfl_xor(l1, off);
-        l2 += __shfl_xor(l2, off);
-        f1 += __shfl_xor(f1, off);
-        f2 += __shfl_xor(f2, off);
-        n1 += __shfl_xor(n1, off);
-        n2 += __shfl_xor(n2, off);
-    }
-    __shared__ double swd[BS / 64][4];
-    __shared__ int swn[BS / 64][2];
-    if (lane == 0) {
-        swd[wid][0] = l1; swd[wid][1] = l2; swd[wid][2] = f1; swd[wid][3] = f2;
-        swn[wid][0] = n1; swn[wid][1] = n2;
-    }
-    __syncthreads();
-    if (tid == 0) {
-        double a0 = 0, a1 = 0, a2 = 0, a3 = 0; int b0 = 0, b1 = 0;
-        for (int wv = 0; wv < BS / 64; wv++) {
-            a0 += swd[wv][0]; a1 += swd[wv][1]; a2 += swd[wv][2]; a3 += swd[wv][3];
-            b0 += swn[wv][0]; b1 += swn[wv][1];
-        }
-        int blk = blockIdx.y * gridDim.x + blockIdx.x;
-        partials[(size_t)blk * 6 + 0] = a0;
-        partials[(size_t)blk * 6 + 1] = a1;
-        partials[(size_t)blk * 6 + 2] = a2;
-        partials[(size_t)blk * 6 + 3] = a3;
-        partials[(size_t)blk * 6 + 4] = (double)b0;
-        partials[(size_t)blk * 6 + 5] = (double)b1;
-    }
-}
-
-__global__ void k_final(const double* __restrict__ partials, int nPart, float* __restrict__ out) {
-    int tid = threadIdx.x;
-    double a[6] = {0, 0, 0, 0, 0, 0};
-    for (int k = tid; k < nPart; k += BS) {
-#pragma unroll
-        for (int j = 0; j < 6; j++) a[j] += partials[(size_t)k * 6 + j];
-    }
-    __shared__ double sd[BS * 6];
-#pragma unroll
-    for (int j = 0; j < 6; j++) sd[tid * 6 + j] = a[j];
-    __syncthreads();
-    for (int s = BS / 2; s > 0; s >>= 1) {
-        if (tid < s) {
-#pragma unroll
-            for (int j = 0; j < 6; j++) sd[tid * 6 + j] += sd[(tid + s) * 6 + j];
-        }
-        __syncthreads();
-    }
-    if (tid == 0) {
-        double L1 = sd[0], L2 = sd[1], F1 = sd[2], F2 = sd[3], N1 = sd[4], N2 = sd[5];
-        double l1v = L1 / fmax(N1, 1.0), l2v = L2 / fmax(N2, 1.0);
-        double f1v = F1 / fmax(N1, 1.0), f2v = F2 / fmax(N2, 1.0);
-        double locl = (N1 > 0 ? l1v : 0.0) + (N2 > 0 ? l2v : 0.0);
-        double clsl = (N1 > 0 ? f1v : 0.0) + (N2 > 0 ? f2v : 0.0);
-        if (N1 == 0 && N2 == 0) { locl = 1e-4; clsl = 1e-4; }
-        out[0] = (float)locl;
-        out[1] = (float)clsl;
     }
 }
 
@@ -567,7 +592,7 @@
     int B = in_sizes[0] / (P * 4);
     int N = in_sizes[3] / (B * 5);
     int C = in_sizes[1] / (B * P);
-    const int CAP = 2048;
+    int CAP = 2048;
     size_t BP = (size_t)B * P;
 
     unsigned char* ws = (unsigned char*)d_ws;
@@ -581,27 +606,35 @@
     float* cand_v = (float*)(ws + alloc((size_t)B * N * CAP * 4));
     int* cand_i = (int*)(ws + alloc((size_t)B * N * CAP * 4));
     int* cand_cnt = (int*)(ws + alloc((size_t)B * N * 4));
-    int bx = (P + BS - 1) / BS;
-    double* partials = (double*)(ws + alloc((size_t)bx * B * 6 * 8));
+    int bxL = (P + BS - 1) / BS;
+    double* partials = (double*)(ws + alloc((size_t)bxL * B * 6 * 8));
     float* out = (float*)d_out;
 
-    hipMemsetAsync(cand_cnt, 0, (size_t)B * N * 4, stream);
-
-    int bxPP = (P + BSK * ILP - 1) / (BSK * ILP);
-    int ngroup = (N + 3) / 4;
-    int bxRM = NSPLIT * ngroup;
-    k_fat1<<<dim3(bxPP + bxRM, B), BSK, 0, stream>>>(loc4, priors4, targets, (float4*)recs,
-                                                     cand_v, cand_i, cand_cnt,
-                                                     part_max, part_arg, P, N, CAP, bxPP);
-
+    int bxPP = (P + BS * ILP - 1) / (BS * ILP);
     int maskWords = (P + 31) / 32;
-    size_t shmem = (size_t)maskWords * 4;
-    k_fat2<<<dim3(N + 1, B), BS, shmem, stream>>>(loc4, priors4, targets,
-                                                  cand_v, cand_i, cand_cnt, tk_s, tk_i,
-                                                  part_max, part_arg, recs, P, N, CAP);
-
-    k_assign<<<dim3(B), BS, 0, stream>>>(targets, tk_s, tk_i, recs, P, N);
-    k_loss<<<dim3(bx, B), BS, 0, stream>>>(loc4, conf, priors4, targets, (const float4*)recs,
-                                           partials, P, N, C);
-    k_final<<<1, BS, 0, stream>>>(partials, bx * B, out);
+    size_t smemBytes = (size_t)maskWords * 4;
+    if (smemBytes < (size_t)BS * KTOP_ * 8) smemBytes = (size_t)BS * KTOP_ * 8;
+    if (smemBytes < (size_t)BS * 6 * 8) smemBytes = (size_t)BS * 6 * 8;
+    if (smemBytes < 6144) smemBytes = 6144;
+
+    int dev = 0;
+    hipGetDevice(&dev);
+    int numCU = 256;
+    hipDeviceGetAttribute(&numCU, hipDeviceAttributeMultiprocessorCount, dev);
+    int blocksPerCU = 0;
+    hipOccupancyMaxActiveBlocksPerMultiprocessor(&blocksPerCU, (const void*)k_mega, BS, smemBytes);
+    if (blocksPerCU < 1) blocksPerCU = 1;
+    int G = numCU * blocksPerCU;
+    int maxWork = bxPP * B + NSPLIT * ((N + 3) / 4) * B;
+    if (G > maxWork) G = maxWork;
+
+    void* args[] = {
+        (void*)&loc4, (void*)&priors4, (void*)&targets, (void*)&conf,
+        (void*)&recs, (void*)&part_max, (void*)&part_arg,
+        (void*)&tk_s, (void*)&tk_i, (void*)&cand_v, (void*)&cand_i, (void*)&cand_cnt,
+        (void*)&partials, (void*)&out,
+        (void*)&P, (void*)&N, (void*)&B, (void*)&C, (void*)&CAP,
+        (void*)&bxPP, (void*)&bxL
+    };
+    hipLaunchCooperativeKernel((const void*)k_mega, dim3(G), dim3(BS), args, (unsigned int)smemBytes, stream);
 }
```

Measured after the change: 665.3 us. 212% more time.
